# Optimization experiments

Hardware: AMD Instinct MI355X
Metric: run time of the kernel (lower is better)

Reference implementation:

```python
import jax, jax.numpy as jnp
import numpy as np

HIDDEN = 1024
N_EXPERTS = 8
TOP_K = 2
INTER = 1408
N_SHARED = 2
SCALE = 1.0  # routed_scaling_factor


def setup_inputs() -> dict:
    key = jax.random.key(0)
    ks = jax.random.split(key, 9)
    s_h = 1.0 / np.sqrt(HIDDEN)
    s_i = 1.0 / np.sqrt(INTER)
    x = jax.random.normal(ks[0], (2, 2048, HIDDEN), dtype=jnp.float32)
    gate_w = jax.random.uniform(ks[1], (N_EXPERTS, HIDDEN), jnp.float32, -s_h, s_h)  # kaiming_uniform-ish
    # routed experts: SwiGLU (gate, up, down), stacked over experts
    wg = jax.random.uniform(ks[2], (N_EXPERTS, HIDDEN, INTER), jnp.float32, -s_h, s_h)
    wu = jax.random.uniform(ks[3], (N_EXPERTS, HIDDEN, INTER), jnp.float32, -s_h, s_h)
    wd = jax.random.uniform(ks[4], (N_EXPERTS, INTER, HIDDEN), jnp.float32, -s_i, s_i)
    # shared experts: one SwiGLU with intermediate = INTER * N_SHARED
    si = INTER * N_SHARED
    s_si = 1.0 / np.sqrt(si)
    swg = jax.random.uniform(ks[5], (HIDDEN, si), jnp.float32, -s_h, s_h)
    swu = jax.random.uniform(ks[6], (HIDDEN, si), jnp.float32, -s_h, s_h)
    swd = jax.random.uniform(ks[7], (si, HIDDEN), jnp.float32, -s_si, s_si)
    return {"x": x, "gate_w": gate_w, "wg": wg, "wu": wu, "wd": wd,
            "swg": swg, "swu": swu, "swd": swd}


def reference(x, gate_w, wg, wu, wd, swg, swu, swd):
    B, S, H = x.shape
    xf = x.reshape(-1, H)                              # [T, H]
    T = xf.shape[0]
    # --- MoEGate (fp32) ---
    logits = xf.astype(jnp.float32) @ gate_w.astype(jnp.float32).T   # [T, E]
    scores = jax.nn.softmax(logits, axis=-1)
    topw, topi = jax.lax.top_k(scores, TOP_K)          # [T, K]
    denom = topw.sum(axis=-1, keepdims=True) + 1e-20   # norm_topk_prob (top_k > 1)
    topw = topw / denom * SCALE
    # dense combine weights [T, E]: zero except at top-k expert slots
    wdense = jnp.zeros((T, N_EXPERTS), jnp.float32).at[
        jnp.arange(T)[:, None], topi].set(topw)
    # --- routed experts (SwiGLU), computed densely per expert and combined ---
    hg = jnp.einsum('th,ehi->eti', xf, wg)             # [E, T, I]
    hu = jnp.einsum('th,ehi->eti', xf, wu)             # [E, T, I]
    eo = jnp.einsum('eti,eih->eth', jax.nn.silu(hg) * hu, wd)   # [E, T, H]
    y = jnp.einsum('te,eth->th', wdense, eo)           # weighted scatter-combine
    # --- shared experts ---
    shared = (jax.nn.silu(xf @ swg) * (xf @ swu)) @ swd
    return (y + shared).reshape(B, S, H)
```

## Files before the change

### kernel.cpp

```cpp
#include <hip/hip_runtime.h>
#include <hip/hip_bf16.h>
#include <math.h>

#define HIDDEN 1024
#define NEXP 8
#define TOPK 2
#define INTER 1408
#define SINTER 2816
#define NTOK 4096
#define NROWS (NTOK * TOPK)
#define NPANEL 10
#define TROWS 16384
#define MAXT 136
#define BPAN (SINTER * HIDDEN)

typedef unsigned short ushort_t;
typedef __attribute__((ext_vector_type(8))) short short8;
typedef __attribute__((ext_vector_type(4))) float f32x4;

__device__ __forceinline__ ushort_t f2bf(float f) {
    unsigned int b = __float_as_uint(f);
    unsigned int r = (b + 0x7FFFu + ((b >> 16) & 1u)) >> 16;
    return (ushort_t)r;
}
__device__ __forceinline__ float bf2f(ushort_t u) {
    return __uint_as_float(((unsigned int)u) << 16);
}
__device__ __forceinline__ float silu_f(float g) {
    return g * (1.0f / (1.0f + __expf(-g)));
}
__device__ __forceinline__ int imin(int a, int b) { return a < b ? a : b; }

#define GLDS16(gp, lp) __builtin_amdgcn_global_load_lds(                     \
    (const __attribute__((address_space(1))) void*)(gp),                     \
    (__attribute__((address_space(3))) void*)(lp), 16, 0, 0)

__global__ void conv_x(const float* __restrict__ src, ushort_t* __restrict__ dst) {
    int i = (blockIdx.x * 256 + threadIdx.x) * 4;
    float4 v = *reinterpret_cast<const float4*>(&src[i]);
    union { ushort_t h[4]; unsigned long long ll; } p;
    p.h[0] = f2bf(v.x); p.h[1] = f2bf(v.y); p.h[2] = f2bf(v.z); p.h[3] = f2bf(v.w);
    *reinterpret_cast<unsigned long long*>(&dst[i]) = p.ll;
}

__global__ __launch_bounds__(256) void tconv64(const float* __restrict__ src,
                                               ushort_t* __restrict__ dst,
                                               int R, int C, long sstride,
                                               long dstride) {
    src += (size_t)blockIdx.z * sstride;
    dst += (size_t)blockIdx.z * dstride;
    __shared__ float tile[32][65];
    int ct = blockIdx.x * 32, rt = blockIdx.y * 64;
    int j = threadIdx.x;
    {
        int r = j >> 2;
        int c0 = (j & 3) * 8;
        const float* s = &src[(size_t)(rt + r) * C + ct + c0];
        float4 v0 = *reinterpret_cast<const float4*>(s);
        float4 v1 = *reinterpret_cast<const float4*>(s + 4);
        tile[c0 + 0][r] = v0.x; tile[c0 + 1][r] = v0.y;
        tile[c0 + 2][r] = v0.z; tile[c0 + 3][r] = v0.w;
        tile[c0 + 4][r] = v1.x; tile[c0 + 5][r] = v1.y;
        tile[c0 + 6][r] = v1.z; tile[c0 + 7][r] = v1.w;
    }
    __syncthreads();
    {
        int c = j >> 3;
        int r0 = (j & 7) * 8;
        union { ushort_t h[8]; short8 v; } p;
#pragma unroll
        for (int i = 0; i < 8; i++) p.h[i] = f2bf(tile[c][r0 + i]);
        *reinterpret_cast<short8*>(&dst[(size_t)(ct + c) * R + rt + r0]) = p.v;
    }
}

__global__ __launch_bounds__(256) void tconv64_gu(const float* __restrict__ src,
                                                  ushort_t* __restrict__ dst,
                                                  int C, long sstride,
                                                  int base_panel, int goff) {
    src += (size_t)blockIdx.z * sstride;
    __shared__ float tile[32][65];
    int ct = blockIdx.x * 32, rt = blockIdx.y * 64;
    int j = threadIdx.x;
    {
        int r = j >> 2;
        int c0 = (j & 3) * 8;
        const float* s = &src[(size_t)(rt + r) * C + ct + c0];
        float4 v0 = *reinterpret_cast<const float4*>(s);
        float4 v1 = *reinterpret_cast<const float4*>(s + 4);
        tile[c0 + 0][r] = v0.x; tile[c0 + 1][r] = v0.y;
        tile[c0 + 2][r] = v0.z; tile[c0 + 3][r] = v0.w;
        tile[c0 + 4][r] = v1.x; tile[c0 + 5][r] = v1.y;
        tile[c0 + 6][r] = v1.z; tile[c0 + 7][r] = v1.w;
    }
    __syncthreads();
    {
        int c = j >> 3;
        int r0 = (j & 7) * 8;
        int gc = ct + c;
        int panel = base_panel + blockIdx.z + gc / INTER;
        int rl = gc % INTER;
        int Rrow = ((rl >> 5) << 6) + (rl & 31) + goff;
        union { ushort_t h[8]; short8 v; } p;
#pragma unroll
        for (int i = 0; i < 8; i++) p.h[i] = f2bf(tile[c][r0 + i]);
        *reinterpret_cast<short8*>(
            &dst[(size_t)panel * BPAN + (size_t)Rrow * HIDDEN + rt + r0]) = p.v;
    }
}

__global__ void gate_kernel(const float* __restrict__ x, const float* __restrict__ gw,
                            int* __restrict__ top_i, float* __restrict__ top_w) {
    int t = blockIdx.x;
    int lane = threadIdx.x;
    const float* xr = x + (size_t)t * HIDDEN;
    float acc[NEXP];
#pragma unroll
    for (int e = 0; e < NEXP; e++) acc[e] = 0.f;
    for (int j = 0; j < HIDDEN / 64; j++) {
        float xv = xr[lane + 64 * j];
#pragma unroll
        for (int e = 0; e < NEXP; e++)
            acc[e] = fmaf(xv, gw[e * HIDDEN + lane + 64 * j], acc[e]);
    }
#pragma unroll
    for (int e = 0; e < NEXP; e++) {
        float v = acc[e];
        for (int off = 32; off > 0; off >>= 1) v += __shfl_xor(v, off, 64);
        acc[e] = v;
    }
    if (lane == 0) {
        float mx = acc[0];
        for (int e = 1; e < NEXP; e++) mx = fmaxf(mx, acc[e]);
        float s[NEXP];
        float sum = 0.f;
        for (int e = 0; e < NEXP; e++) { s[e] = __expf(acc[e] - mx); sum += s[e]; }
        float inv = 1.0f / sum;
        for (int e = 0; e < NEXP; e++) s[e] *= inv;
        int e0 = 0;
        for (int e = 1; e < NEXP; e++) if (s[e] > s[e0]) e0 = e;
        int e1 = -1;
        for (int e = 0; e < NEXP; e++) {
            if (e == e0) continue;
            if (e1 < 0 || s[e] > s[e1]) e1 = e;
        }
        float w0 = s[e0], w1 = s[e1];
        float denom = w0 + w1 + 1e-20f;
        top_i[t * 2 + 0] = e0;
        top_i[t * 2 + 1] = e1;
        top_w[t * 2 + 0] = w0 / denom;
        top_w[t * 2 + 1] = w1 / denom;
    }
}

__global__ void assign_kernel(const int* __restrict__ top_i, int* __restrict__ cnt,
                              int* __restrict__ rnk) {
    int j = blockIdx.x * blockDim.x + threadIdx.x;
    if (j < NROWS) rnk[j] = atomicAdd(&cnt[top_i[j]], 1);
}

__global__ void scan_kernel(const int* __restrict__ cnt, int* __restrict__ offs2,
                            int* __restrict__ cnt2, int* __restrict__ task_pm) {
    if (threadIdx.x == 0) {
        int o = 0;
        for (int e = 0; e < NEXP; e++) { offs2[e] = o; cnt2[e] = cnt[e]; o += cnt[e]; }
        offs2[8] = NROWS;          cnt2[8] = NTOK;
        offs2[9] = NROWS + NTOK;   cnt2[9] = NTOK;
        offs2[10] = TROWS;
        int t = 0;
        for (int e = 0; e < NPANEL; e++)
            for (int m0 = 0; m0 < cnt2[e]; m0 += 128)
                task_pm[t++] = (e << 16) | (m0 >> 7);
        for (; t < MAXT; t++) task_pm[t] = -1;
    }
}

__global__ void fill_kernel(const int* __restrict__ top_i, const float* __restrict__ top_w,
                            const int* __restrict__ rnk, const int* __restrict__ offs2,
                            int* __restrict__ tok_of_row, float* __restrict__ w_of_row,
                            int* __restrict__ inv_row) {
    int j = blockIdx.x * blockDim.x + threadIdx.x;
    if (j < NROWS) {
        int row = offs2[top_i[j]] + rnk[j];
        tok_of_row[row] = j;
        w_of_row[row] = top_w[j];
        inv_row[j] = row;
    }
}

__global__ void fill_shared(int* __restrict__ tok_of_row) {
    int j = blockIdx.x * blockDim.x + threadIdx.x;
    tok_of_row[NROWS + j] = (j & (NTOK - 1)) << 1;
}

__global__ __launch_bounds__(256, 4) void gemm_gu(
    const ushort_t* __restrict__ xb, const ushort_t* __restrict__ Bhat,
    ushort_t* __restrict__ act, const int* __restrict__ tok_of_row,
    const int* __restrict__ offs2, const int* __restrict__ cnt2,
    const int* __restrict__ task_pm) {
    int T = gridDim.x;
    int orig = blockIdx.x;
    int logical = (orig & 7) * (T >> 3) + (orig >> 3);
    int task = logical % MAXT;
    int nidx = logical / MAXT;
    int tk = task_pm[task];
    if (tk < 0) return;
    int e = tk >> 16;
    int m0 = (tk & 0xffff) << 7;
    int mcnt = cnt2[e];
    int base = offs2[e];
    int n0 = nidx * 128;
    const ushort_t* B = Bhat + (size_t)e * BPAN;

    __shared__ short As[8 * 1024];
    __shared__ short Bs[8 * 1024];

    int tid = threadIdx.x;
    int wave = tid >> 6, lane = tid & 63;
    int wr = wave >> 1, wc = wave & 1;
    int lr = lane & 15;
    int kq = (lane >> 4) * 8;

    int r0 = m0 + 32 * wave + lr, r1 = r0 + 16;
    int rr0 = base + imin(r0, mcnt - 1);
    int rr1 = base + imin(r1, mcnt - 1);
    const ushort_t* srcA0 = xb + (size_t)(tok_of_row[rr0] >> 1) * HIDDEN + kq;
    const ushort_t* srcA1 = xb + (size_t)(tok_of_row[rr1] >> 1) * HIDDEN + kq;
    const ushort_t* srcB0 = B + (size_t)(n0 + 32 * wave + lr) * HIDDEN + kq;
    const ushort_t* srcB1 = srcB0 + (size_t)16 * HIDDEN;

    f32x4 acc[4][4] = {};

    for (int k0 = 0; k0 < HIDDEN; k0 += 64) {
        GLDS16(srcA0 + k0,      &As[(2 * wave) * 1024]);
        GLDS16(srcA0 + k0 + 32, &As[(2 * wave) * 1024 + 512]);
        GLDS16(srcA1 + k0,      &As[(2 * wave + 1) * 1024]);
        GLDS16(srcA1 + k0 + 32, &As[(2 * wave + 1) * 1024 + 512]);
        GLDS16(srcB0 + k0,      &Bs[(2 * wave) * 1024]);
        GLDS16(srcB0 + k0 + 32, &Bs[(2 * wave) * 1024 + 512]);
        GLDS16(srcB1 + k0,      &Bs[(2 * wave + 1) * 1024]);
        GLDS16(srcB1 + k0 + 32, &Bs[(2 * wave + 1) * 1024 + 512]);
        __syncthreads();
#pragma unroll
        for (int s = 0; s < 2; s++) {
            short8 a[4], b[4];
#pragma unroll
            for (int mi = 0; mi < 4; mi++)
                a[mi] = *reinterpret_cast<const short8*>(
                    &As[(wr * 4 + mi) * 1024 + s * 512 + lane * 8]);
#pragma unroll
            for (int ni = 0; ni < 4; ni++)
                b[ni] = *reinterpret_cast<const short8*>(
                    &Bs[(wc * 4 + ni) * 1024 + s * 512 + lane * 8]);
#pragma unroll
            for (int mi = 0; mi < 4; mi++)
#pragma unroll
                for (int ni = 0; ni < 4; ni++)
                    acc[mi][ni] = __builtin_amdgcn_mfma_f32_16x16x32_bf16(
                        a[mi], b[ni], acc[mi][ni], 0, 0, 0);
        }
        __syncthreads();
    }

    int colbase = 32 * ((n0 >> 6) + wc);
#pragma unroll
    for (int mi = 0; mi < 4; mi++) {
#pragma unroll
        for (int r = 0; r < 4; r++) {
            int gm = m0 + wr * 64 + mi * 16 + (lane >> 4) * 4 + r;
            if (gm < mcnt) {
#pragma unroll
                for (int ni = 0; ni < 2; ni++) {
                    float g = acc[mi][ni][r], u = acc[mi][ni + 2][r];
                    act[(size_t)(base + gm) * INTER + colbase + ni * 16 + lr] =
                        f2bf(silu_f(g) * u);
                }
            }
        }
    }
}

__global__ __launch_bounds__(256, 2) void gemm_down(
    const ushort_t* __restrict__ act, const ushort_t* __restrict__ WdT,
    ushort_t* __restrict__ part, const int* __restrict__ offs2,
    const int* __restrict__ cnt2, const int* __restrict__ task_pm) {
    int T = gridDim.x;
    int orig = blockIdx.x;
    int logical = (orig & 7) * (T >> 3) + (orig >> 3);
    int task = logical % MAXT;
    int nidx = logical / MAXT;
    int tk = task_pm[task];
    if (tk < 0) return;
    int e = tk >> 16;
    int m0 = (tk & 0xffff) << 7;
    int mcnt = cnt2[e];
    int base = offs2[e];
    int n0 = nidx * 256;
    const ushort_t* Bd = WdT + (size_t)e * HIDDEN * INTER;

    __shared__ short As[8 * 1024];
    __shared__ short Bs[16 * 1024];

    int tid = threadIdx.x;
    int wave = tid >> 6, lane = tid & 63;
    int wr = wave >> 1, wc = wave & 1;
    int lr = lane & 15;
    int kq = (lane >> 4) * 8;

    const ushort_t* srcA0 = act + (size_t)(base + m0 + 32 * wave + lr) * INTER + kq;
    const ushort_t* srcA1 = srcA0 + (size_t)16 * INTER;
    const ushort_t* srcB0 = Bd + (size_t)(n0 + 64 * wave + lr) * INTER + kq;
    const ushort_t* srcB1 = srcB0 + (size_t)16 * INTER;
    const ushort_t* srcB2 = srcB0 + (size_t)32 * INTER;
    const ushort_t* srcB3 = srcB0 + (size_t)48 * INTER;

    f32x4 acc[4][8] = {};

    for (int k0 = 0; k0 < INTER; k0 += 64) {
        GLDS16(srcA0 + k0,      &As[(2 * wave) * 1024]);
        GLDS16(srcA0 + k0 + 32, &As[(2 * wave) * 1024 + 512]);
        GLDS16(srcA1 + k0,      &As[(2 * wave + 1) * 1024]);
        GLDS16(srcA1 + k0 + 32, &As[(2 * wave + 1) * 1024 + 512]);
        GLDS16(srcB0 + k0,      &Bs[(4 * wave) * 1024]);
        GLDS16(srcB0 + k0 + 32, &Bs[(4 * wave) * 1024 + 512]);
        GLDS16(srcB1 + k0,      &Bs[(4 * wave + 1) * 1024]);
        GLDS16(srcB1 + k0 + 32, &Bs[(4 * wave + 1) * 1024 + 512]);
        GLDS16(srcB2 + k0,      &Bs[(4 * wave + 2) * 1024]);
        GLDS16(srcB2 + k0 + 32, &Bs[(4 * wave + 2) * 1024 + 512]);
        GLDS16(srcB3 + k0,      &Bs[(4 * wave + 3) * 1024]);
        GLDS16(srcB3 + k0 + 32, &Bs[(4 * wave + 3) * 1024 + 512]);
        __syncthreads();
#pragma unroll
        for (int s = 0; s < 2; s++) {
            short8 a[4], b[8];
#pragma unroll
            for (int mi = 0; mi < 4; mi++)
                a[mi] = *reinterpret_cast<const short8*>(
                    &As[(wr * 4 + mi) * 1024 + s * 512 + lane * 8]);
#pragma unroll
            for (int ni = 0; ni < 8; ni++)
                b[ni] = *reinterpret_cast<const short8*>(
                    &Bs[(wc * 8 + ni) * 1024 + s * 512 + lane * 8]);
#pragma unroll
            for (int mi = 0; mi < 4; mi++)
#pragma unroll
                for (int ni = 0; ni < 8; ni++)
                    acc[mi][ni] = __builtin_amdgcn_mfma_f32_16x16x32_bf16(
                        a[mi], b[ni], acc[mi][ni], 0, 0, 0);
        }
        __syncthreads();
    }

#pragma unroll
    for (int mi = 0; mi < 4; mi++) {
#pragma unroll
        for (int r = 0; r < 4; r++) {
            int gm = m0 + wr * 64 + mi * 16 + (lane >> 4) * 4 + r;
            if (gm < mcnt) {
#pragma unroll
                for (int ni = 0; ni < 8; ni++) {
                    int col = n0 + wc * 128 + ni * 16 + lr;
                    part[(size_t)(base + gm) * HIDDEN + col] = f2bf(acc[mi][ni][r]);
                }
            }
        }
    }
}

__global__ __launch_bounds__(256) void combine_kernel(
    const ushort_t* __restrict__ part, const int* __restrict__ inv_row,
    const float* __restrict__ w_of_row, float* __restrict__ out) {
    int t = blockIdx.x;
    int c = threadIdx.x * 4;
    int r0 = inv_row[2 * t], r1 = inv_row[2 * t + 1];
    float w0 = w_of_row[r0], w1 = w_of_row[r1];
    ushort4 a0 = *reinterpret_cast<const ushort4*>(&part[(size_t)r0 * HIDDEN + c]);
    ushort4 a1 = *reinterpret_cast<const ushort4*>(&part[(size_t)r1 * HIDDEN + c]);
    ushort4 a2 = *reinterpret_cast<const ushort4*>(&part[((size_t)NROWS + t) * HIDDEN + c]);
    ushort4 a3 = *reinterpret_cast<const ushort4*>(&part[((size_t)NROWS + NTOK + t) * HIDDEN + c]);
    float4 o;
    o.x = w0 * bf2f(a0.x) + w1 * bf2f(a1.x) + bf2f(a2.x) + bf2f(a3.x);
    o.y = w0 * bf2f(a0.y) + w1 * bf2f(a1.y) + bf2f(a2.y) + bf2f(a3.y);
    o.z = w0 * bf2f(a0.z) + w1 * bf2f(a1.z) + bf2f(a2.z) + bf2f(a3.z);
    o.w = w0 * bf2f(a0.w) + w1 * bf2f(a1.w) + bf2f(a2.w) + bf2f(a3.w);
    *reinterpret_cast<float4*>(&out[(size_t)t * HIDDEN + c]) = o;
}

extern "C" void kernel_launch(void* const* d_in, const int* in_sizes, int n_in,
                              void* d_out, int out_size, void* d_ws, size_t ws_size,
                              hipStream_t stream) {
    const float* x   = (const float*)d_in[0];
    const float* gw  = (const float*)d_in[1];
    const float* wg  = (const float*)d_in[2];
    const float* wu  = (const float*)d_in[3];
    const float* wd  = (const float*)d_in[4];
    const float* swg = (const float*)d_in[5];
    const float* swu = (const float*)d_in[6];
    const float* swd = (const float*)d_in[7];
    float* out = (float*)d_out;

    const size_t XB   = (size_t)NTOK * HIDDEN;
    const size_t BHAT = (size_t)NPANEL * BPAN;
    const size_t WDT  = (size_t)NPANEL * INTER * HIDDEN;
    const size_t ACT  = (size_t)TROWS * INTER;
    const size_t PART = (size_t)TROWS * HIDDEN;
    ushort_t* xb   = (ushort_t*)d_ws;
    ushort_t* bhat = xb + XB;
    ushort_t* wdT  = bhat + BHAT;
    ushort_t* act  = wdT + WDT;
    ushort_t* part = act + ACT;
    int* ib = (int*)(part + PART);
    int* top_i      = ib;
    int* rnk        = ib + NROWS;
    int* cnt        = ib + 2 * NROWS;
    int* offs2      = ib + 2 * NROWS + 8;
    int* cnt2       = offs2 + 16;
    int* task_pm    = cnt2 + 16;
    int* tok_of_row = task_pm + MAXT;
    int* inv_row    = tok_of_row + TROWS;
    float* top_w    = (float*)(inv_row + NROWS);
    float* w_of_row = top_w + NROWS;

    conv_x<<<(NTOK * HIDDEN) / (256 * 4), 256, 0, stream>>>(x, xb);
    tconv64_gu<<<dim3(INTER / 32, HIDDEN / 64, NEXP), 256, 0, stream>>>(
        wg, bhat, INTER, (long)HIDDEN * INTER, 0, 0);
    tconv64_gu<<<dim3(INTER / 32, HIDDEN / 64, NEXP), 256, 0, stream>>>(
        wu, bhat, INTER, (long)HIDDEN * INTER, 0, 32);
    tconv64_gu<<<dim3(SINTER / 32, HIDDEN / 64, 1), 256, 0, stream>>>(
        swg, bhat, SINTER, 0, 8, 0);
    tconv64_gu<<<dim3(SINTER / 32, HIDDEN / 64, 1), 256, 0, stream>>>(
        swu, bhat, SINTER, 0, 8, 32);
    tconv64<<<dim3(HIDDEN / 32, INTER / 64, NEXP), 256, 0, stream>>>(
        wd, wdT, INTER, HIDDEN, (long)INTER * HIDDEN, (long)HIDDEN * INTER);
    tconv64<<<dim3(HIDDEN / 32, INTER / 64, 2), 256, 0, stream>>>(
        swd, wdT + (size_t)8 * HIDDEN * INTER, INTER, HIDDEN,
        (long)INTER * HIDDEN, (long)HIDDEN * INTER);

    gate_kernel<<<NTOK, 64, 0, stream>>>(x, gw, top_i, top_w);
    hipMemsetAsync(cnt, 0, 8 * sizeof(int), stream);
    assign_kernel<<<NROWS / 256, 256, 0, stream>>>(top_i, cnt, rnk);
    scan_kernel<<<1, 1, 0, stream>>>(cnt, offs2, cnt2, task_pm);
    fill_kernel<<<NROWS / 256, 256, 0, stream>>>(top_i, top_w, rnk, offs2,
                                                 tok_of_row, w_of_row, inv_row);
    fill_shared<<<NROWS / 256, 256, 0, stream>>>(tok_of_row);

    gemm_gu<<<MAXT * (SINTER / 128), 256, 0, stream>>>(
        xb, bhat, act, tok_of_row, offs2, cnt2, task_pm);
    gemm_down<<<MAXT * (HIDDEN / 256), 256, 0, stream>>>(
        act, wdT, part, offs2, cnt2, task_pm);
    combine_kernel<<<NTOK, 256, 0, stream>>>(part, inv_row, w_of_row, out);
}
```

Measured before the change: 435.6 us.

## Rewrite gate/up GEMM as 256x256 tile with double-buffered LDS pipeline

Rebuilds the gate/up grouped GEMM around 512-thread blocks computing 256x256 tiles, with a new 256-row task list built in the scan kernel. LDS is double-buffered and the next k-slab is prefetched with global_load_lds in chunks interleaved between MFMA groups, using explicit vmcnt waits, sched barriers and setprio. The goal is to hide global-load latency behind MFMA work and raise data reuse per block. In exchange there is one block per CU, more padding waste from the coarser 256-row tiles on uneven expert counts, and fragile hand-tuned wait counts.

```diff
diff --git a/kernel.cpp b/kernel.cpp
--- a/kernel.cpp
+++ b/kernel.cpp
@@ -12,6 +12,7 @@
 #define NPANEL 10
 #define TROWS 16384
 #define MAXT 136
+#define MAXT2 72
 #define BPAN (SINTER * HIDDEN)
 
 typedef unsigned short ushort_t;
@@ -34,6 +35,12 @@
 #define GLDS16(gp, lp) __builtin_amdgcn_global_load_lds(                     \
     (const __attribute__((address_space(1))) void*)(gp),                     \
     (__attribute__((address_space(3))) void*)(lp), 16, 0, 0)
+
+#define SBAR do {                                                            \
+        __builtin_amdgcn_sched_barrier(0);                                   \
+        __builtin_amdgcn_s_barrier();                                        \
+        __builtin_amdgcn_sched_barrier(0);                                   \
+    } while (0)
 
 __global__ void conv_x(const float* __restrict__ src, ushort_t* __restrict__ dst) {
     int i = (blockIdx.x * 256 + threadIdx.x) * 4;
@@ -160,7 +167,8 @@
 }
 
 __global__ void scan_kernel(const int* __restrict__ cnt, int* __restrict__ offs2,
-                            int* __restrict__ cnt2, int* __restrict__ task_pm) {
+                            int* __restrict__ cnt2, int* __restrict__ task_pm,
+                            int* __restrict__ task256) {
     if (threadIdx.x == 0) {
         int o = 0;
         for (int e = 0; e < NEXP; e++) { offs2[e] = o; cnt2[e] = cnt[e]; o += cnt[e]; }
@@ -172,6 +180,11 @@
             for (int m0 = 0; m0 < cnt2[e]; m0 += 128)
                 task_pm[t++] = (e << 16) | (m0 >> 7);
         for (; t < MAXT; t++) task_pm[t] = -1;
+        int u = 0;
+        for (int e = 0; e < NPANEL; e++)
+            for (int m0 = 0; m0 < cnt2[e]; m0 += 256)
+                task256[u++] = (e << 16) | (m0 >> 8);
+        for (; u < MAXT2; u++) task256[u] = -1;
     }
 }
 
@@ -193,86 +206,131 @@
     tok_of_row[NROWS + j] = (j & (NTOK - 1)) << 1;
 }
 
-__global__ __launch_bounds__(256, 4) void gemm_gu(
+__global__ __launch_bounds__(512, 1) void gemm_gu(
     const ushort_t* __restrict__ xb, const ushort_t* __restrict__ Bhat,
     ushort_t* __restrict__ act, const int* __restrict__ tok_of_row,
     const int* __restrict__ offs2, const int* __restrict__ cnt2,
-    const int* __restrict__ task_pm) {
+    const int* __restrict__ task256) {
     int T = gridDim.x;
     int orig = blockIdx.x;
     int logical = (orig & 7) * (T >> 3) + (orig >> 3);
-    int task = logical % MAXT;
-    int nidx = logical / MAXT;
-    int tk = task_pm[task];
+    int task = logical % MAXT2;
+    int nidx = logical / MAXT2;
+    int tk = task256[task];
     if (tk < 0) return;
     int e = tk >> 16;
-    int m0 = (tk & 0xffff) << 7;
+    int m0 = (tk & 0xffff) << 8;
     int mcnt = cnt2[e];
     int base = offs2[e];
-    int n0 = nidx * 128;
+    int n0h = nidx * 256;
     const ushort_t* B = Bhat + (size_t)e * BPAN;
 
-    __shared__ short As[8 * 1024];
-    __shared__ short Bs[8 * 1024];
+    __shared__ short As[2][2][16][512];
+    __shared__ short Bs[2][2][16][512];
 
     int tid = threadIdx.x;
     int wave = tid >> 6, lane = tid & 63;
-    int wr = wave >> 1, wc = wave & 1;
+    int wm = wave >> 2, wn = wave & 3;
     int lr = lane & 15;
     int kq = (lane >> 4) * 8;
 
-    int r0 = m0 + 32 * wave + lr, r1 = r0 + 16;
-    int rr0 = base + imin(r0, mcnt - 1);
-    int rr1 = base + imin(r1, mcnt - 1);
+    int ar0 = 16 * (2 * wave) + lr, ar1 = ar0 + 16;
+    int rr0 = base + imin(m0 + ar0, mcnt - 1);
+    int rr1 = base + imin(m0 + ar1, mcnt - 1);
     const ushort_t* srcA0 = xb + (size_t)(tok_of_row[rr0] >> 1) * HIDDEN + kq;
     const ushort_t* srcA1 = xb + (size_t)(tok_of_row[rr1] >> 1) * HIDDEN + kq;
-    const ushort_t* srcB0 = B + (size_t)(n0 + 32 * wave + lr) * HIDDEN + kq;
+    const ushort_t* srcB0 = B + (size_t)(n0h + 16 * (2 * wave) + lr) * HIDDEN + kq;
     const ushort_t* srcB1 = srcB0 + (size_t)16 * HIDDEN;
 
-    f32x4 acc[4][4] = {};
-
-    for (int k0 = 0; k0 < HIDDEN; k0 += 64) {
-        GLDS16(srcA0 + k0,      &As[(2 * wave) * 1024]);
-        GLDS16(srcA0 + k0 + 32, &As[(2 * wave) * 1024 + 512]);
-        GLDS16(srcA1 + k0,      &As[(2 * wave + 1) * 1024]);
-        GLDS16(srcA1 + k0 + 32, &As[(2 * wave + 1) * 1024 + 512]);
-        GLDS16(srcB0 + k0,      &Bs[(2 * wave) * 1024]);
-        GLDS16(srcB0 + k0 + 32, &Bs[(2 * wave) * 1024 + 512]);
-        GLDS16(srcB1 + k0,      &Bs[(2 * wave + 1) * 1024]);
-        GLDS16(srcB1 + k0 + 32, &Bs[(2 * wave + 1) * 1024 + 512]);
-        __syncthreads();
-#pragma unroll
-        for (int s = 0; s < 2; s++) {
-            short8 a[4], b[4];
-#pragma unroll
-            for (int mi = 0; mi < 4; mi++)
-                a[mi] = *reinterpret_cast<const short8*>(
-                    &As[(wr * 4 + mi) * 1024 + s * 512 + lane * 8]);
-#pragma unroll
-            for (int ni = 0; ni < 4; ni++)
-                b[ni] = *reinterpret_cast<const short8*>(
-                    &Bs[(wc * 4 + ni) * 1024 + s * 512 + lane * 8]);
-#pragma unroll
-            for (int mi = 0; mi < 4; mi++)
-#pragma unroll
-                for (int ni = 0; ni < 4; ni++)
-                    acc[mi][ni] = __builtin_amdgcn_mfma_f32_16x16x32_bf16(
-                        a[mi], b[ni], acc[mi][ni], 0, 0, 0);
-        }
-        __syncthreads();
-    }
-
-    int colbase = 32 * ((n0 >> 6) + wc);
-#pragma unroll
-    for (int mi = 0; mi < 4; mi++) {
+    f32x4 acc[8][4] = {};
+
+#define SGA(d, s, kk) do {                                                   \
+        GLDS16(srcA0 + (kk) + (s) * 32, &As[d][s][2 * wave][0]);             \
+        GLDS16(srcA1 + (kk) + (s) * 32, &As[d][s][2 * wave + 1][0]);         \
+    } while (0)
+#define SGB(d, s, kk) do {                                                   \
+        GLDS16(srcB0 + (kk) + (s) * 32, &Bs[d][s][2 * wave][0]);             \
+        GLDS16(srcB1 + (kk) + (s) * 32, &Bs[d][s][2 * wave + 1][0]);         \
+    } while (0)
+
+    SGA(0, 0, 0); SGB(0, 0, 0); SGA(0, 1, 0); SGB(0, 1, 0);
+    SGA(1, 0, 64); SGB(1, 0, 64); SGA(1, 1, 64); SGB(1, 1, 64);
+
+    const int NT = HIDDEN / 64;
+    short8 a[8], b0, b1, b2, b3;
+    for (int t = 0; t < NT; t++) {
+        int d = t & 1;
+        int kk1 = (t + 1) * 64, kk2 = (t + 2) * 64;
+        bool st1 = (t >= 1) && (t + 1 < NT);
+        bool st2 = (t + 2 < NT);
+        if (t == 0)           asm volatile("s_waitcnt vmcnt(8)" ::: "memory");
+        else if (t == NT - 1) asm volatile("s_waitcnt vmcnt(0)" ::: "memory");
+        else                  asm volatile("s_waitcnt vmcnt(4)" ::: "memory");
+        SBAR;
+#pragma unroll
+        for (int m = 0; m < 8; m++)
+            a[m] = *reinterpret_cast<const short8*>(&As[d][0][wm * 8 + m][lane * 8]);
+        b0 = *reinterpret_cast<const short8*>(&Bs[d][0][wn * 4 + 0][lane * 8]);
+        b1 = *reinterpret_cast<const short8*>(&Bs[d][0][wn * 4 + 1][lane * 8]);
+        if (st1) SGA(d ^ 1, 1, kk1);
+        __builtin_amdgcn_s_setprio(1);
+#pragma unroll
+        for (int m = 0; m < 8; m++) {
+            acc[m][0] = __builtin_amdgcn_mfma_f32_16x16x32_bf16(a[m], b0, acc[m][0], 0, 0, 0);
+            acc[m][1] = __builtin_amdgcn_mfma_f32_16x16x32_bf16(a[m], b1, acc[m][1], 0, 0, 0);
+        }
+        __builtin_amdgcn_s_setprio(0);
+        SBAR;
+        b2 = *reinterpret_cast<const short8*>(&Bs[d][0][wn * 4 + 2][lane * 8]);
+        b3 = *reinterpret_cast<const short8*>(&Bs[d][0][wn * 4 + 3][lane * 8]);
+        if (st1) SGB(d ^ 1, 1, kk1);
+        __builtin_amdgcn_s_setprio(1);
+#pragma unroll
+        for (int m = 0; m < 8; m++) {
+            acc[m][2] = __builtin_amdgcn_mfma_f32_16x16x32_bf16(a[m], b2, acc[m][2], 0, 0, 0);
+            acc[m][3] = __builtin_amdgcn_mfma_f32_16x16x32_bf16(a[m], b3, acc[m][3], 0, 0, 0);
+        }
+        __builtin_amdgcn_s_setprio(0);
+        SBAR;
+#pragma unroll
+        for (int m = 0; m < 8; m++)
+            a[m] = *reinterpret_cast<const short8*>(&As[d][1][wm * 8 + m][lane * 8]);
+        b0 = *reinterpret_cast<const short8*>(&Bs[d][1][wn * 4 + 0][lane * 8]);
+        b1 = *reinterpret_cast<const short8*>(&Bs[d][1][wn * 4 + 1][lane * 8]);
+        if (st2) SGA(d, 0, kk2);
+        __builtin_amdgcn_s_setprio(1);
+#pragma unroll
+        for (int m = 0; m < 8; m++) {
+            acc[m][0] = __builtin_amdgcn_mfma_f32_16x16x32_bf16(a[m], b0, acc[m][0], 0, 0, 0);
+            acc[m][1] = __builtin_amdgcn_mfma_f32_16x16x32_bf16(a[m], b1, acc[m][1], 0, 0, 0);
+        }
+        __builtin_amdgcn_s_setprio(0);
+        SBAR;
+        b2 = *reinterpret_cast<const short8*>(&Bs[d][1][wn * 4 + 2][lane * 8]);
+        b3 = *reinterpret_cast<const short8*>(&Bs[d][1][wn * 4 + 3][lane * 8]);
+        if (st2) SGB(d, 0, kk2);
+        __builtin_amdgcn_s_setprio(1);
+#pragma unroll
+        for (int m = 0; m < 8; m++) {
+            acc[m][2] = __builtin_amdgcn_mfma_f32_16x16x32_bf16(a[m], b2, acc[m][2], 0, 0, 0);
+            acc[m][3] = __builtin_amdgcn_mfma_f32_16x16x32_bf16(a[m], b3, acc[m][3], 0, 0, 0);
+        }
+        __builtin_amdgcn_s_setprio(0);
+    }
+#undef SGA
+#undef SGB
+
+    int colbase = 32 * (nidx * 4 + wn);
+#pragma unroll
+    for (int m = 0; m < 8; m++) {
 #pragma unroll
         for (int r = 0; r < 4; r++) {
-            int gm = m0 + wr * 64 + mi * 16 + (lane >> 4) * 4 + r;
+            int gm = m0 + wm * 128 + m * 16 + (lane >> 4) * 4 + r;
             if (gm < mcnt) {
 #pragma unroll
-                for (int ni = 0; ni < 2; ni++) {
-                    float g = acc[mi][ni][r], u = acc[mi][ni + 2][r];
-                    act[(size_t)(base + gm) * INTER + colbase + ni * 16 + lr] =
+                for (int n = 0; n < 2; n++) {
+                    float g = acc[m][n][r], u = acc[m][n + 2][r];
+                    act[(size_t)(base + gm) * INTER + colbase + n * 16 + lr] =
                         f2bf(silu_f(g) * u);
                 }
             }
@@ -416,7 +474,8 @@
     int* offs2      = ib + 2 * NROWS + 8;
     int* cnt2       = offs2 + 16;
     int* task_pm    = cnt2 + 16;
-    int* tok_of_row = task_pm + MAXT;
+    int* task256    = task_pm + MAXT;
+    int* tok_of_row = task256 + MAXT2;
     int* inv_row    = tok_of_row + TROWS;
     float* top_w    = (float*)(inv_row + NROWS);
     float* w_of_row = top_w + NROWS;
@@ -439,13 +498,13 @@
     gate_kernel<<<NTOK, 64, 0, stream>>>(x, gw, top_i, top_w);
     hipMemsetAsync(cnt, 0, 8 * sizeof(int), stream);
     assign_kernel<<<NROWS / 256, 256, 0, stream>>>(top_i, cnt, rnk);
-    scan_kernel<<<1, 1, 0, stream>>>(cnt, offs2, cnt2, task_pm);
+    scan_kernel<<<1, 1, 0, stream>>>(cnt, offs2, cnt2, task_pm, task256);
     fill_kernel<<<NROWS / 256, 256, 0, stream>>>(top_i, top_w, rnk, offs2,
                                                  tok_of_row, w_of_row, inv_row);
     fill_shared<<<NROWS / 256, 256, 0, stream>>>(tok_of_row);
 
-    gemm_gu<<<MAXT * (SINTER / 128), 256, 0, stream>>>(
-        xb, bhat, act, tok_of_row, offs2, cnt2, task_pm);
+    gemm_gu<<<MAXT2 * (SINTER / 256), 512, 0, stream>>>(
+        xb, bhat, act, tok_of_row, offs2, cnt2, task256);
     gemm_down<<<MAXT * (HIDDEN / 256), 256, 0, stream>>>(
         act, wdT, part, offs2, cnt2, task_pm);
     combine_kernel<<<NTOK, 256, 0, stream>>>(part, inv_row, w_of_row, out);
```

New measurement: 390.4 us. -10.4%, faster.
